# Performance work log

Hardware: AMD Instinct MI355X
Metric: run time of the kernel (lower is better)

The kernel has to match this reference:

```python
import jax, jax.numpy as jnp
import numpy as np

H = 2048      # hidden_size
I = 768       # moe_intermediate_size
E = 32        # num_experts
K = 4         # num_experts_per_tok
B, S = 1, 2048


def setup_inputs() -> dict:
    key = jax.random.key(0)
    k0, k1, k2, k3, k4 = jax.random.split(key, 5)
    return {
        "hidden_states": jax.random.normal(k0, (B, S, H), dtype=jnp.float32),
        "gate_w": jax.random.normal(k1, (E, H), dtype=jnp.float32) * 0.02,
        "Wg": jax.random.normal(k2, (E, H, I), dtype=jnp.float32) * 0.02,
        "Wu": jax.random.normal(k3, (E, H, I), dtype=jnp.float32) * 0.02,
        "Wd": jax.random.normal(k4, (E, I, H), dtype=jnp.float32) * 0.02,
        "top_k": K,
    }


def reference(hidden_states, gate_w, Wg, Wu, Wd, top_k):
    b, s, h = hidden_states.shape
    x = hidden_states.reshape(-1, h)                      # [T, H]
    T = x.shape[0]
    e = gate_w.shape[0]

    # Router: softmax over experts, then top-k and renormalize (norm_topk_prob=True)
    logits = x @ gate_w.T                                 # [T, E]
    probs = jax.nn.softmax(logits, axis=-1)
    w, sel = jax.lax.top_k(probs, top_k)                  # [T, K]
    w = w / jnp.sum(w, axis=-1, keepdims=True)

    # Scatter top-k weights into a dense [T, E] combine matrix
    combine = jnp.zeros((T, e), dtype=x.dtype).at[
        jnp.arange(T)[:, None], sel].add(w)               # [T, E]

    # Expert SiLU-gated MLPs, computed densely for all experts (mirrors the
    # ttnn path that repeats tokens across local experts and masks on combine)
    g = jnp.einsum('th,ehi->eti', x, Wg)                  # [E, T, I]
    u = jnp.einsum('th,ehi->eti', x, Wu)                  # [E, T, I]
    a = jax.nn.silu(g) * u                                # [E, T, I]
    # Fold combine weights in before the down projection to avoid an [E,T,H] temp
    a = a * combine.T[:, :, None]                         # [E, T, I]
    out = jnp.einsum('eti,eih->th', a, Wd)                # [T, H]
    return out.reshape(b, s, h)
```

## Files before the change

### kernel.cpp

```cpp
#include <hip/hip_runtime.h>
#include <cstdint>
#include <cstddef>

#define TDIM 2048
#define HDIM 2048
#define IDIM 768
#define EXP  32
#define TOPK 4
#define TKTOT 8192
#define MAXMETA 96

typedef __attribute__((ext_vector_type(8))) short short8;
typedef __attribute__((ext_vector_type(4))) float f32x4;

constexpr size_t OFF_XBF = 0;
constexpr size_t OFF_ACT = OFF_XBF + (size_t)TDIM * HDIM * 2;
constexpr size_t OFF_LOG = OFF_ACT + (size_t)TKTOT * IDIM * 2;
constexpr size_t OFF_SEL = OFF_LOG + (size_t)TDIM * EXP * 4;
constexpr size_t OFF_WTS = OFF_SEL + (size_t)TDIM * TOPK * 4;
constexpr size_t OFF_STK = OFF_WTS + (size_t)TDIM * TOPK * 4;
constexpr size_t OFF_SW  = OFF_STK + (size_t)TKTOT * 4;
constexpr size_t OFF_INV = OFF_SW  + (size_t)TKTOT * 4;
constexpr size_t OFF_CNT = OFF_INV + (size_t)TDIM * TOPK * 4;
constexpr size_t OFF_CUR = OFF_CNT + EXP * 4;
constexpr size_t OFF_OFS = OFF_CUR + EXP * 4;
constexpr size_t OFF_MET = OFF_OFS + (EXP + 1) * 4;
constexpr size_t OFF_NB  = OFF_MET + MAXMETA * 2 * 4;
constexpr size_t OFF_TMP = (OFF_NB + 4 + 255) & ~(size_t)255;
constexpr size_t TMP_BYTES = (size_t)TKTOT * HDIM * 4;
constexpr size_t WB_BYTES = (size_t)EXP * HDIM * IDIM * 2;
constexpr size_t OFF_WGB = (OFF_TMP + TMP_BYTES + 255) & ~(size_t)255;
constexpr size_t OFF_WUB = OFF_WGB + WB_BYTES;
constexpr size_t OFF_WDB = OFF_WUB + WB_BYTES;
constexpr size_t NEED_BF = OFF_WDB + WB_BYTES;

__device__ __forceinline__ unsigned short f2bf(float f) {
  unsigned u = __float_as_uint(f);
  u = (u + 0x7fffu + ((u >> 16) & 1u)) >> 16;
  return (unsigned short)u;
}
__device__ __forceinline__ unsigned pk2(float a, float b) {
  return (unsigned)f2bf(a) | ((unsigned)f2bf(b) << 16);
}
__device__ __forceinline__ void async16(void* lds, const void* g) {
  __builtin_amdgcn_global_load_lds((const __attribute__((address_space(1))) void*)g,
                                   (__attribute__((address_space(3))) void*)lds, 16, 0, 0);
}

__global__ __launch_bounds__(256) void k_cvt(const float* __restrict__ x,
                                             unsigned short* __restrict__ xb) {
  int i = blockIdx.x * 256 + threadIdx.x;
  const float4* s = (const float4*)x;
  float4 a = s[2 * i], b = s[2 * i + 1];
  uint4 o;
  o.x = pk2(a.x, a.y); o.y = pk2(a.z, a.w);
  o.z = pk2(b.x, b.y); o.w = pk2(b.z, b.w);
  ((uint4*)xb)[i] = o;
}

__global__ __launch_bounds__(256) void k_trw(const float* __restrict__ src,
                                             unsigned short* __restrict__ dst,
                                             int R, int C) {
  __shared__ float sm[64 * 65];
  int t = threadIdx.x;
  int c0 = blockIdx.x * 64, r0 = blockIdx.y * 64;
  size_t base = (size_t)blockIdx.z * R * C;
  const float* s = src + base + (size_t)r0 * C + c0;
#pragma unroll
  for (int p = 0; p < 4; p++) {
    int rl = p * 16 + (t >> 4), cl = (t & 15) * 4;
    float4 v = *(const float4*)(s + (size_t)rl * C + cl);
    float* d = &sm[rl * 65 + cl];
    d[0] = v.x; d[1] = v.y; d[2] = v.z; d[3] = v.w;
  }
  __syncthreads();
  unsigned short* o = dst + base + (size_t)c0 * R + r0;
#pragma unroll
  for (int q = 0; q < 4; q++) {
    int cl = q * 16 + (t >> 4), rq = (t & 15) * 4;
    float v0 = sm[(rq + 0) * 65 + cl], v1 = sm[(rq + 1) * 65 + cl];
    float v2 = sm[(rq + 2) * 65 + cl], v3 = sm[(rq + 3) * 65 + cl];
    uint2 u; u.x = pk2(v0, v1); u.y = pk2(v2, v3);
    *(uint2*)(o + (size_t)cl * R + rq) = u;
  }
}

__global__ __launch_bounds__(256) void k_router(const float* __restrict__ x,
                                                const float* __restrict__ gw,
                                                float* __restrict__ logits) {
  __shared__ float smx[4 * HDIM];
  int tid = threadIdx.x;
  int t0 = blockIdx.x * 4;
  const float4* src = (const float4*)(x + (size_t)t0 * HDIM);
  float4* dst = (float4*)smx;
#pragma unroll
  for (int i = 0; i < 8; i++) dst[i * 256 + tid] = src[i * 256 + tid];
  __syncthreads();
  int e = tid >> 3, sl = tid & 7;
  float acc[4] = {0.f, 0.f, 0.f, 0.f};
  const float* gptr = gw + (size_t)e * HDIM + sl * 256;
#pragma unroll 4
  for (int j = 0; j < 64; j++) {
    float4 g4 = *(const float4*)(gptr + j * 4);
#pragma unroll
    for (int tt = 0; tt < 4; tt++) {
      float4 xa = *(const float4*)&smx[tt * HDIM + sl * 256 + j * 4];
      acc[tt] += g4.x * xa.x + g4.y * xa.y + g4.z * xa.z + g4.w * xa.w;
    }
  }
  __syncthreads();
#pragma unroll
  for (int tt = 0; tt < 4; tt++) smx[(tt * EXP + e) * 8 + sl] = acc[tt];
  __syncthreads();
  if (tid < 128) {
    int tt = tid >> 5, ee = tid & 31;
    float s = 0.f;
#pragma unroll
    for (int q = 0; q < 8; q++) s += smx[(tt * EXP + ee) * 8 + q];
    logits[(size_t)(t0 + tt) * EXP + ee] = s;
  }
}

__global__ __launch_bounds__(256) void k_topk(const float* __restrict__ logits,
                                              int* __restrict__ sel,
                                              float* __restrict__ wts,
                                              int* __restrict__ cnt) {
  int t = blockIdx.x * 256 + threadIdx.x;
  float p[EXP];
  float mx = -1e30f;
#pragma unroll
  for (int e = 0; e < EXP; e++) { p[e] = logits[(size_t)t * EXP + e]; mx = fmaxf(mx, p[e]); }
#pragma unroll
  for (int e = 0; e < EXP; e++) p[e] = __expf(p[e] - mx);
  unsigned used = 0; int si[TOPK]; float sv[TOPK]; float tot = 0.f;
  for (int k = 0; k < TOPK; k++) {
    float bm = -1.f; int bi = 0;
#pragma unroll
    for (int e = 0; e < EXP; e++) {
      bool ok = !((used >> e) & 1) && (p[e] > bm);
      bm = ok ? p[e] : bm;
      bi = ok ? e : bi;
    }
    used |= 1u << bi; si[k] = bi; sv[k] = bm; tot += bm;
  }
  float inv = 1.f / tot;
#pragma unroll
  for (int k = 0; k < TOPK; k++) {
    sel[t * TOPK + k] = si[k];
    wts[t * TOPK + k] = sv[k] * inv;
    atomicAdd(&cnt[si[k]], 1);
  }
}

__global__ void k_scan(const int* __restrict__ cnt, int* __restrict__ offs,
                       int* __restrict__ cur, int* __restrict__ meta,
                       int* __restrict__ nb) {
  if (threadIdx.x == 0 && blockIdx.x == 0) {
    int off = 0, n = 0;
    for (int e = 0; e < EXP; e++) {
      offs[e] = off; cur[e] = off;
      int c = cnt[e];
      for (int r = 0; r < c && n < MAXMETA; r += 128) { meta[n * 2] = e; meta[n * 2 + 1] = r; n++; }
      off += c;
    }
    offs[EXP] = off;
    nb[0] = n;
  }
}

__global__ __launch_bounds__(256) void k_scatter(const int* __restrict__ sel,
                                                 const float* __restrict__ wts,
                                                 int* __restrict__ cur,
                                                 int* __restrict__ stok,
                                                 float* __restrict__ sw,
                                                 int* __restrict__ inv) {
  int t = blockIdx.x * 256 + threadIdx.x;
#pragma unroll
  for (int k = 0; k < TOPK; k++) {
    int e = sel[t * TOPK + k];
    int p = atomicAdd(&cur[e], 1);
    stok[p] = t;
    sw[p] = wts[t * TOPK + k];
    inv[t * TOPK + k] = p;
  }
}

__global__ __launch_bounds__(256, 3) void k_gemm1b(
    const unsigned short* __restrict__ Wgb, const unsigned short* __restrict__ Wub,
    const unsigned short* __restrict__ xb,
    const int* __restrict__ stok, const float* __restrict__ sw,
    const int* __restrict__ cnt, const int* __restrict__ offs,
    const int* __restrict__ meta, const int* __restrict__ nb,
    unsigned short* __restrict__ act) {
  int bid = blockIdx.x;
  if (bid >= nb[0]) return;
  int e = meta[bid * 2], r0 = meta[bid * 2 + 1];
  int pos0 = offs[e] + r0;
  int rows = min(128, cnt[e] - r0);
  int n0 = blockIdx.y * 64;

  __shared__ unsigned short smA[128 * 64];
  __shared__ unsigned short smBg[64 * 64];
  __shared__ unsigned short smBu[64 * 64];
  __shared__ int smTok[128];
  __shared__ float smW[128];

  int tid = threadIdx.x;
  if (tid < 128) {
    int rr = (tid < rows) ? tid : 0;
    smTok[tid] = stok[pos0 + rr];
    smW[tid] = (tid < rows) ? sw[pos0 + tid] : 0.f;
  }
  __syncthreads();

  int lane = tid & 63, w = tid >> 6;
  int waveM = w >> 1, waveN = w & 1;

  const unsigned short* aP[4];
  unsigned short* aD[4];
#pragma unroll
  for (int p = 0; p < 4; p++) {
    int r = p * 32 + w * 8 + (lane >> 3);
    aP[p] = xb + (size_t)smTok[r] * HDIM + (((lane & 7) ^ (r & 7)) << 3);
    aD[p] = &smA[(p * 32 + w * 8) * 64];
  }
  const unsigned short* gP[2]; unsigned short* gD[2];
  const unsigned short* uP[2]; unsigned short* uD[2];
  size_t wbase = (size_t)e * IDIM * HDIM;
#pragma unroll
  for (int p = 0; p < 2; p++) {
    int nr = p * 32 + w * 8 + (lane >> 3);
    size_t go = wbase + (size_t)(n0 + nr) * HDIM + (((lane & 7) ^ (nr & 7)) << 3);
    gP[p] = Wgb + go; uP[p] = Wub + go;
    gD[p] = &smBg[(p * 32 + w * 8) * 64];
    uD[p] = &smBu[(p * 32 + w * 8) * 64];
  }

  f32x4 accG[4][2], accU[4][2];
#pragma unroll
  for (int a = 0; a < 4; a++)
#pragma unroll
    for (int b = 0; b < 2; b++) { accG[a][b] = {0.f,0.f,0.f,0.f}; accU[a][b] = {0.f,0.f,0.f,0.f}; }

  int lm = lane & 15, lq = lane >> 4;

  for (int kt = 0; kt < HDIM / 64; kt++) {
    __syncthreads();
#pragma unroll
    for (int p = 0; p < 4; p++) async16(aD[p], aP[p]);
#pragma unroll
    for (int p = 0; p < 2; p++) async16(gD[p], gP[p]);
#pragma unroll
    for (int p = 0; p < 2; p++) async16(uD[p], uP[p]);
    __syncthreads();
#pragma unroll
    for (int s = 0; s < 2; s++) {
      int kq = s * 4 + lq;
      short8 af[4], bg[2], bu[2];
#pragma unroll
      for (int mt = 0; mt < 4; mt++) {
        int m = waveM * 64 + mt * 16 + lm;
        af[mt] = *(const short8*)&smA[m * 64 + ((kq ^ (m & 7)) << 3)];
      }
#pragma unroll
      for (int nt = 0; nt < 2; nt++) {
        int n = waveN * 32 + nt * 16 + lm;
        int off = n * 64 + ((kq ^ (n & 7)) << 3);
        bg[nt] = *(const short8*)&smBg[off];
        bu[nt] = *(const short8*)&smBu[off];
      }
#pragma unroll
      for (int mt = 0; mt < 4; mt++)
#pragma unroll
        for (int nt = 0; nt < 2; nt++) {
          accG[mt][nt] = __builtin_amdgcn_mfma_f32_16x16x32_bf16(af[mt], bg[nt], accG[mt][nt], 0, 0, 0);
          accU[mt][nt] = __builtin_amdgcn_mfma_f32_16x16x32_bf16(af[mt], bu[nt], accU[mt][nt], 0, 0, 0);
        }
    }
#pragma unroll
    for (int p = 0; p < 4; p++) aP[p] += 64;
#pragma unroll
    for (int p = 0; p < 2; p++) { gP[p] += 64; uP[p] += 64; }
  }

#pragma unroll
  for (int mt = 0; mt < 4; mt++)
#pragma unroll
    for (int nt = 0; nt < 2; nt++) {
      int n = n0 + waveN * 32 + nt * 16 + lm;
#pragma unroll
      for (int i = 0; i < 4; i++) {
        int r = waveM * 64 + mt * 16 + lq * 4 + i;
        if (r < rows) {
          float g = accG[mt][nt][i], u = accU[mt][nt][i];
          float sg = g / (1.f + __expf(-g));
          act[(size_t)(pos0 + r) * IDIM + n] = f2bf(sg * u * smW[r]);
        }
      }
    }
}

__global__ __launch_bounds__(256, 3) void k_gemm2b(
    const unsigned short* __restrict__ Wdb, const unsigned short* __restrict__ act,
    const int* __restrict__ cnt, const int* __restrict__ offs,
    const int* __restrict__ meta, const int* __restrict__ nb,
    float* __restrict__ tmp) {
  int bid = blockIdx.x;
  if (bid >= nb[0]) return;
  int e = meta[bid * 2], r0 = meta[bid * 2 + 1];
  int pos0 = offs[e] + r0;
  int rows = min(128, cnt[e] - r0);
  int n0 = blockIdx.y * 128;

  __shared__ unsigned short smA[128 * 64];
  __shared__ unsigned short smB[128 * 64];

  int tid = threadIdx.x;
  int lane = tid & 63, w = tid >> 6;
  int waveM = w >> 1, waveN = w & 1;

  const unsigned short* aP[4];
  unsigned short* aD[4];
#pragma unroll
  for (int p = 0; p < 4; p++) {
    int r = p * 32 + w * 8 + (lane >> 3);
    int pp = pos0 + r; if (pp > TKTOT - 1) pp = TKTOT - 1;
    aP[p] = act + (size_t)pp * IDIM + (((lane & 7) ^ (r & 7)) << 3);
    aD[p] = &smA[(p * 32 + w * 8) * 64];
  }
  const unsigned short* bP[4]; unsigned short* bD[4];
  size_t wbase = (size_t)e * IDIM * HDIM;
#pragma unroll
  for (int p = 0; p < 4; p++) {
    int nr = p * 32 + w * 8 + (lane >> 3);
    bP[p] = Wdb + wbase + (size_t)(n0 + nr) * IDIM + (((lane & 7) ^ (nr & 7)) << 3);
    bD[p] = &smB[(p * 32 + w * 8) * 64];
  }

  f32x4 acc[4][4];
#pragma unroll
  for (int a = 0; a < 4; a++)
#pragma unroll
    for (int b = 0; b < 4; b++) acc[a][b] = {0.f, 0.f, 0.f, 0.f};

  int lm = lane & 15, lq = lane >> 4;

  for (int kt = 0; kt < IDIM / 64; kt++) {
    __syncthreads();
#pragma unroll
    for (int p = 0; p < 4; p++) async16(aD[p], aP[p]);
#pragma unroll
    for (int p = 0; p < 4; p++) async16(bD[p], bP[p]);
    __syncthreads();
#pragma unroll
    for (int s = 0; s < 2; s++) {
      int kq = s * 4 + lq;
      short8 af[4], bf[4];
#pragma unroll
      for (int mt = 0; mt < 4; mt++) {
        int m = waveM * 64 + mt * 16 + lm;
        af[mt] = *(const short8*)&smA[m * 64 + ((kq ^ (m & 7)) << 3)];
      }
#pragma unroll
      for (int nt = 0; nt < 4; nt++) {
        int n = waveN * 64 + nt * 16 + lm;
        bf[nt] = *(const short8*)&smB[n * 64 + ((kq ^ (n & 7)) << 3)];
      }
#pragma unroll
      for (int mt = 0; mt < 4; mt++)
#pragma unroll
        for (int nt = 0; nt < 4; nt++)
          acc[mt][nt] = __builtin_amdgcn_mfma_f32_16x16x32_bf16(af[mt], bf[nt], acc[mt][nt], 0, 0, 0);
    }
#pragma unroll
    for (int p = 0; p < 4; p++) { aP[p] += 64; bP[p] += 64; }
  }

#pragma unroll
  for (int mt = 0; mt < 4; mt++)
#pragma unroll
    for (int nt = 0; nt < 4; nt++) {
      int n = n0 + waveN * 64 + nt * 16 + lm;
#pragma unroll
      for (int i = 0; i < 4; i++) {
        int r = waveM * 64 + mt * 16 + lq * 4 + i;
        if (r < rows) tmp[(size_t)(pos0 + r) * HDIM + n] = acc[mt][nt][i];
      }
    }
}

__global__ __launch_bounds__(256, 2) void k_gemm1(
    const float* __restrict__ Wg, const float* __restrict__ Wu,
    const unsigned short* __restrict__ xb,
    const int* __restrict__ stok, const float* __restrict__ sw,
    const int* __restrict__ cnt, const int* __restrict__ offs,
    const int* __restrict__ meta, const int* __restrict__ nb,
    unsigned short* __restrict__ act) {
  int bid = blockIdx.x;
  if (bid >= nb[0]) return;
  int e = meta[bid * 2 + 0];
  int r0 = meta[bid * 2 + 1];
  int pos0 = offs[e] + r0;
  int rows = min(128, cnt[e] - r0);
  int n0 = blockIdx.y * 128;

  __shared__ unsigned short smA[128 * 64];
  __shared__ unsigned short smBg[128 * 64];
  __shared__ unsigned short smBu[128 * 64];
  __shared__ int smTok[128];
  __shared__ float smW[128];

  int tid = threadIdx.x;
  if (tid < 128) {
    int r = tid;
    int rr = (r < rows) ? r : 0;
    smTok[r] = stok[pos0 + rr];
    smW[r] = (r < rows) ? sw[pos0 + r] : 0.f;
  }
  __syncthreads();

  int lane = tid & 63, w = tid >> 6;
  int waveM = w >> 1, waveN = w & 1;

  const unsigned short* aP[4];
  unsigned short* aD[4];
#pragma unroll
  for (int p = 0; p < 4; p++) {
    int r = p * 32 + w * 8 + (lane >> 3);
    aP[p] = xb + (size_t)smTok[r] * HDIM + (((lane & 7) ^ (r & 7)) << 3);
    aD[p] = &smA[(p * 32 + w * 8) * 64];
  }
  int bn = tid & 127, kh = tid >> 7;
  const float* pG = Wg + (size_t)e * HDIM * IDIM + (size_t)(kh * 32) * IDIM + n0 + bn;
  const float* pU = Wu + (size_t)e * HDIM * IDIM + (size_t)(kh * 32) * IDIM + n0 + bn;

  f32x4 accG[4][4], accU[4][4];
#pragma unroll
  for (int a = 0; a < 4; a++)
#pragma unroll
    for (int b = 0; b < 4; b++) { accG[a][b] = {0.f,0.f,0.f,0.f}; accU[a][b] = {0.f,0.f,0.f,0.f}; }

  int lm = lane & 15, lq = lane >> 4;

  for (int kt = 0; kt < HDIM / 64; kt++) {
    __syncthreads();
#pragma unroll
    for (int p = 0; p < 4; p++) async16(aD[p], aP[p]);
    {
      const float* q = pG; float v[32];
#pragma unroll
      for (int j = 0; j < 32; j++) { v[j] = *q; q += IDIM; }
#pragma unroll
      for (int jj = 0; jj < 4; jj++) {
        short8 o;
#pragma unroll
        for (int z = 0; z < 8; z++) o[z] = (short)f2bf(v[jj * 8 + z]);
        int ck = kh * 4 + jj;
        *(short8*)&smBg[bn * 64 + ((ck ^ (bn & 7)) << 3)] = o;
      }
    }
    {
      const float* q = pU; float v[32];
#pragma unroll
      for (int j = 0; j < 32; j++) { v[j] = *q; q += IDIM; }
#pragma unroll
      for (int jj = 0; jj < 4; jj++) {
        short8 o;
#pragma unroll
        for (int z = 0; z < 8; z++) o[z] = (short)f2bf(v[jj * 8 + z]);
        int ck = kh * 4 + jj;
        *(short8*)&smBu[bn * 64 + ((ck ^ (bn & 7)) << 3)] = o;
      }
    }
    __syncthreads();
#pragma unroll
    for (int s = 0; s < 2; s++) {
      int kq = s * 4 + lq;
      short8 af[4], bg[4], bu[4];
#pragma unroll
      for (int mt = 0; mt < 4; mt++) {
        int m = waveM * 64 + mt * 16 + lm;
        af[mt] = *(const short8*)&smA[m * 64 + ((kq ^ (m & 7)) << 3)];
      }
#pragma unroll
      for (int nt = 0; nt < 4; nt++) {
        int n = waveN * 64 + nt * 16 + lm;
        int off = n * 64 + ((kq ^ (n & 7)) << 3);
        bg[nt] = *(const short8*)&smBg[off];
        bu[nt] = *(const short8*)&smBu[off];
      }
#pragma unroll
      for (int mt = 0; mt < 4; mt++)
#pragma unroll
        for (int nt = 0; nt < 4; nt++) {
          accG[mt][nt] = __builtin_amdgcn_mfma_f32_16x16x32_bf16(af[mt], bg[nt], accG[mt][nt], 0, 0, 0);
          accU[mt][nt] = __builtin_amdgcn_mfma_f32_16x16x32_bf16(af[mt], bu[nt], accU[mt][nt], 0, 0, 0);
        }
    }
#pragma unroll
    for (int p = 0; p < 4; p++) aP[p] += 64;
    pG += (size_t)64 * IDIM;
    pU += (size_t)64 * IDIM;
  }

#pragma unroll
  for (int mt = 0; mt < 4; mt++)
#pragma unroll
    for (int nt = 0; nt < 4; nt++) {
      int n = n0 + waveN * 64 + nt * 16 + lm;
#pragma unroll
      for (int i = 0; i < 4; i++) {
        int r = waveM * 64 + mt * 16 + lq * 4 + i;
        if (r < rows) {
          float g = accG[mt][nt][i], u = accU[mt][nt][i];
          float sg = g / (1.f + __expf(-g));
          act[(size_t)(pos0 + r) * IDIM + n] = f2bf(sg * u * smW[r]);
        }
      }
    }
}

__global__ __launch_bounds__(256, 2) void k_gemm2(
    const float* __restrict__ Wd, const unsigned short* __restrict__ act,
    const int* __restrict__ stok, const int* __restrict__ cnt,
    const int* __restrict__ offs, const int* __restrict__ meta,
    const int* __restrict__ nb, float* __restrict__ dst, int mode) {
  int bid = blockIdx.x;
  if (bid >= nb[0]) return;
  int e = meta[bid * 2 + 0];
  int r0 = meta[bid * 2 + 1];
  int pos0 = offs[e] + r0;
  int rows = min(128, cnt[e] - r0);
  int n0 = blockIdx.y * 128;

  __shared__ unsigned short smA[128 * 64];
  __shared__ unsigned short smB[128 * 64];
  __shared__ int smTok[128];

  int tid = threadIdx.x;
  if (tid < 128) {
    int r = tid;
    int rr = (r < rows) ? r : 0;
    smTok[r] = stok[pos0 + rr];
  }
  __syncthreads();

  int lane = tid & 63, w = tid >> 6;
  int waveM = w >> 1, waveN = w & 1;

  const unsigned short* aP[4];
  unsigned short* aD[4];
#pragma unroll
  for (int p = 0; p < 4; p++) {
    int r = p * 32 + w * 8 + (lane >> 3);
    int pp = pos0 + r; if (pp > TKTOT - 1) pp = TKTOT - 1;
    aP[p] = act + (size_t)pp * IDIM + (((lane & 7) ^ (r & 7)) << 3);
    aD[p] = &smA[(p * 32 + w * 8) * 64];
  }
  int bn = tid & 127, kh = tid >> 7;
  const float* pD = Wd + (size_t)e * IDIM * HDIM + (size_t)(kh * 32) * HDIM + n0 + bn;

  f32x4 acc[4][4];
#pragma unroll
  for (int a = 0; a < 4; a++)
#pragma unroll
    for (int b = 0; b < 4; b++) acc[a][b] = {0.f, 0.f, 0.f, 0.f};

  int lm = lane & 15, lq = lane >> 4;

  for (int kt = 0; kt < IDIM / 64; kt++) {
    __syncthreads();
#pragma unroll
    for (int p = 0; p < 4; p++) async16(aD[p], aP[p]);
    {
      const float* q = pD; float v[32];
#pragma unroll
      for (int j = 0; j < 32; j++) { v[j] = *q; q += HDIM; }
#pragma unroll
      for (int jj = 0; jj < 4; jj++) {
        short8 o;
#pragma unroll
        for (int z = 0; z < 8; z++) o[z] = (short)f2bf(v[jj * 8 + z]);
        int ck = kh * 4 + jj;
        *(short8*)&smB[bn * 64 + ((ck ^ (bn & 7)) << 3)] = o;
      }
    }
    __syncthreads();
#pragma unroll
    for (int s = 0; s < 2; s++) {
      int kq = s * 4 + lq;
      short8 af[4], bf[4];
#pragma unroll
      for (int mt = 0; mt < 4; mt++) {
        int m = waveM * 64 + mt * 16 + lm;
        af[mt] = *(const short8*)&smA[m * 64 + ((kq ^ (m & 7)) << 3)];
      }
#pragma unroll
      for (int nt = 0; nt < 4; nt++) {
        int n = waveN * 64 + nt * 16 + lm;
        bf[nt] = *(const short8*)&smB[n * 64 + ((kq ^ (n & 7)) << 3)];
      }
#pragma unroll
      for (int mt = 0; mt < 4; mt++)
#pragma unroll
        for (int nt = 0; nt < 4; nt++)
          acc[mt][nt] = __builtin_amdgcn_mfma_f32_16x16x32_bf16(af[mt], bf[nt], acc[mt][nt], 0, 0, 0);
    }
#pragma unroll
    for (int p = 0; p < 4; p++) aP[p] += 64;
    pD += (size_t)64 * HDIM;
  }

#pragma unroll
  for (int mt = 0; mt < 4; mt++)
#pragma unroll
    for (int nt = 0; nt < 4; nt++) {
      int n = n0 + waveN * 64 + nt * 16 + lm;
#pragma unroll
      for (int i = 0; i < 4; i++) {
        int r = waveM * 64 + mt * 16 + lq * 4 + i;
        if (r < rows) {
          float val = acc[mt][nt][i];
          if (mode == 0) {
            dst[(size_t)(pos0 + r) * HDIM + n] = val;
          } else {
            __hip_atomic_fetch_add(&dst[(size_t)smTok[r] * HDIM + n], val,
                                   __ATOMIC_RELAXED, __HIP_MEMORY_SCOPE_AGENT);
          }
        }
      }
    }
}

__global__ __launch_bounds__(256) void k_reduce(const float* __restrict__ tmp,
                                                const int* __restrict__ inv,
                                                float* __restrict__ out) {
  int u = blockIdx.x * 256 + threadIdx.x;
  int t = u >> 9, c = u & 511;
  int i0 = inv[t * 4 + 0], i1 = inv[t * 4 + 1], i2 = inv[t * 4 + 2], i3 = inv[t * 4 + 3];
  float4 a = *(const float4*)(tmp + (size_t)i0 * HDIM + c * 4);
  float4 b = *(const float4*)(tmp + (size_t)i1 * HDIM + c * 4);
  float4 d = *(const float4*)(tmp + (size_t)i2 * HDIM + c * 4);
  float4 e = *(const float4*)(tmp + (size_t)i3 * HDIM + c * 4);
  float4 s;
  s.x = a.x + b.x + d.x + e.x;
  s.y = a.y + b.y + d.y + e.y;
  s.z = a.z + b.z + d.z + e.z;
  s.w = a.w + b.w + d.w + e.w;
  *(float4*)(out + (size_t)t * HDIM + c * 4) = s;
}

extern "C" void kernel_launch(void* const* d_in, const int* in_sizes, int n_in,
                              void* d_out, int out_size, void* d_ws, size_t ws_size,
                              hipStream_t stream) {
  const float* x  = (const float*)d_in[0];
  const float* gw = (const float*)d_in[1];
  const float* Wg = (const float*)d_in[2];
  const float* Wu = (const float*)d_in[3];
  const float* Wd = (const float*)d_in[4];
  float* out = (float*)d_out;

  char* ws = (char*)d_ws;
  unsigned short* xb  = (unsigned short*)(ws + OFF_XBF);
  unsigned short* act = (unsigned short*)(ws + OFF_ACT);
  float* logits = (float*)(ws + OFF_LOG);
  int*   sel    = (int*)(ws + OFF_SEL);
  float* wts    = (float*)(ws + OFF_WTS);
  int*   stok   = (int*)(ws + OFF_STK);
  float* sw     = (float*)(ws + OFF_SW);
  int*   inv    = (int*)(ws + OFF_INV);
  int*   cnt    = (int*)(ws + OFF_CNT);
  int*   cur    = (int*)(ws + OFF_CUR);
  int*   offs   = (int*)(ws + OFF_OFS);
  int*   meta   = (int*)(ws + OFF_MET);
  int*   nb     = (int*)(ws + OFF_NB);
  float* tmp    = (float*)(ws + OFF_TMP);
  unsigned short* Wgb = (unsigned short*)(ws + OFF_WGB);
  unsigned short* Wub = (unsigned short*)(ws + OFF_WUB);
  unsigned short* Wdb = (unsigned short*)(ws + OFF_WDB);

  bool useTmp = ws_size >= OFF_TMP + TMP_BYTES;
  bool useBF  = ws_size >= NEED_BF;

  hipMemsetAsync(cnt, 0, EXP * 4, stream);
  k_cvt<<<(TDIM * HDIM / 8) / 256, 256, 0, stream>>>(x, xb);
  k_router<<<TDIM / 4, 256, 0, stream>>>(x, gw, logits);
  k_topk<<<TDIM / 256, 256, 0, stream>>>(logits, sel, wts, cnt);
  k_scan<<<1, 64, 0, stream>>>(cnt, offs, cur, meta, nb);
  k_scatter<<<TDIM / 256, 256, 0, stream>>>(sel, wts, cur, stok, sw, inv);

  if (useBF) {
    k_trw<<<dim3(IDIM / 64, HDIM / 64, EXP), 256, 0, stream>>>(Wg, Wgb, HDIM, IDIM);
    k_trw<<<dim3(IDIM / 64, HDIM / 64, EXP), 256, 0, stream>>>(Wu, Wub, HDIM, IDIM);
    k_trw<<<dim3(HDIM / 64, IDIM / 64, EXP), 256, 0, stream>>>(Wd, Wdb, IDIM, HDIM);
    k_gemm1b<<<dim3(MAXMETA, IDIM / 64), 256, 0, stream>>>(Wgb, Wub, xb, stok, sw, cnt, offs, meta, nb, act);
    k_gemm2b<<<dim3(MAXMETA, HDIM / 128), 256, 0, stream>>>(Wdb, act, cnt, offs, meta, nb, tmp);
    k_reduce<<<(TDIM * 512) / 256, 256, 0, stream>>>(tmp, inv, out);
  } else {
    k_gemm1<<<dim3(MAXMETA, IDIM / 128), 256, 0, stream>>>(Wg, Wu, xb, stok, sw, cnt, offs, meta, nb, act);
    if (useTmp) {
      k_gemm2<<<dim3(MAXMETA, HDIM / 128), 256, 0, stream>>>(Wd, act, stok, cnt, offs, meta, nb, tmp, 0);
      k_reduce<<<(TDIM * 512) / 256, 256, 0, stream>>>(tmp, inv, out);
    } else {
      hipMemsetAsync(out, 0, (size_t)TDIM * HDIM * 4, stream);
      k_gemm2<<<dim3(MAXMETA, HDIM / 128), 256, 0, stream>>>(Wd, act, stok, cnt, offs, meta, nb, out, 1);
    }
  }
}
```

Baseline: 828.4 us.

## Drop weight pre-transpose; stream fp32 weights into double-buffered 256-row expert GEMMs

Removes the per-call kernels that transposed all expert weights to bf16 in workspace. The two grouped GEMMs now read fp32 weights directly and convert them to bf16 in registers. Both GEMMs get double-buffered LDS, with the next tile's loads issued before the current tile's MFMAs. Tiles grow to 256 tokens with 512-thread blocks, and block indices are remapped. The aim is to cut the extra full pass over weight memory and to hide load latency, at the cost of uncoalesced strided fp32 weight loads, more register and LDS pressure, and one block per CU.

```diff
diff --git a/kernel.cpp b/kernel.cpp
--- a/kernel.cpp
+++ b/kernel.cpp
@@ -9,6 +9,8 @@
 #define TOPK 4
 #define TKTOT 8192
 #define MAXMETA 96
+#define CHUNK 256
+#define NMETA 64
 
 typedef __attribute__((ext_vector_type(8))) short short8;
 typedef __attribute__((ext_vector_type(4))) float f32x4;
@@ -28,11 +30,6 @@
 constexpr size_t OFF_NB  = OFF_MET + MAXMETA * 2 * 4;
 constexpr size_t OFF_TMP = (OFF_NB + 4 + 255) & ~(size_t)255;
 constexpr size_t TMP_BYTES = (size_t)TKTOT * HDIM * 4;
-constexpr size_t WB_BYTES = (size_t)EXP * HDIM * IDIM * 2;
-constexpr size_t OFF_WGB = (OFF_TMP + TMP_BYTES + 255) & ~(size_t)255;
-constexpr size_t OFF_WUB = OFF_WGB + WB_BYTES;
-constexpr size_t OFF_WDB = OFF_WUB + WB_BYTES;
-constexpr size_t NEED_BF = OFF_WDB + WB_BYTES;
 
 __device__ __forceinline__ unsigned short f2bf(float f) {
   unsigned u = __float_as_uint(f);
@@ -58,33 +55,6 @@
   ((uint4*)xb)[i] = o;
 }
 
-__global__ __launch_bounds__(256) void k_trw(const float* __restrict__ src,
-                                             unsigned short* __restrict__ dst,
-                                             int R, int C) {
-  __shared__ float sm[64 * 65];
-  int t = threadIdx.x;
-  int c0 = blockIdx.x * 64, r0 = blockIdx.y * 64;
-  size_t base = (size_t)blockIdx.z * R * C;
-  const float* s = src + base + (size_t)r0 * C + c0;
-#pragma unroll
-  for (int p = 0; p < 4; p++) {
-    int rl = p * 16 + (t >> 4), cl = (t & 15) * 4;
-    float4 v = *(const float4*)(s + (size_t)rl * C + cl);
-    float* d = &sm[rl * 65 + cl];
-    d[0] = v.x; d[1] = v.y; d[2] = v.z; d[3] = v.w;
-  }
-  __syncthreads();
-  unsigned short* o = dst + base + (size_t)c0 * R + r0;
-#pragma unroll
-  for (int q = 0; q < 4; q++) {
-    int cl = q * 16 + (t >> 4), rq = (t & 15) * 4;
-    float v0 = sm[(rq + 0) * 65 + cl], v1 = sm[(rq + 1) * 65 + cl];
-    float v2 = sm[(rq + 2) * 65 + cl], v3 = sm[(rq + 3) * 65 + cl];
-    uint2 u; u.x = pk2(v0, v1); u.y = pk2(v2, v3);
-    *(uint2*)(o + (size_t)cl * R + rq) = u;
-  }
-}
-
 __global__ __launch_bounds__(256) void k_router(const float* __restrict__ x,
                                                 const float* __restrict__ gw,
                                                 float* __restrict__ logits) {
@@ -160,7 +130,7 @@
     for (int e = 0; e < EXP; e++) {
       offs[e] = off; cur[e] = off;
       int c = cnt[e];
-      for (int r = 0; r < c && n < MAXMETA; r += 128) { meta[n * 2] = e; meta[n * 2 + 1] = r; n++; }
+      for (int r = 0; r < c && n < NMETA; r += CHUNK) { meta[n * 2] = e; meta[n * 2 + 1] = r; n++; }
       off += c;
     }
     offs[EXP] = off;
@@ -185,28 +155,28 @@
   }
 }
 
-__global__ __launch_bounds__(256, 3) void k_gemm1b(
-    const unsigned short* __restrict__ Wgb, const unsigned short* __restrict__ Wub,
+__global__ __launch_bounds__(512, 1) void k_gemm1n(
+    const float* __restrict__ Wg, const float* __restrict__ Wu,
     const unsigned short* __restrict__ xb,
     const int* __restrict__ stok, const float* __restrict__ sw,
     const int* __restrict__ cnt, const int* __restrict__ offs,
     const int* __restrict__ meta, const int* __restrict__ nb,
     unsigned short* __restrict__ act) {
-  int bid = blockIdx.x;
+  int bid = (blockIdx.x & 7) * 8 + (blockIdx.x >> 3);
   if (bid >= nb[0]) return;
   int e = meta[bid * 2], r0 = meta[bid * 2 + 1];
   int pos0 = offs[e] + r0;
-  int rows = min(128, cnt[e] - r0);
+  int rows = min(CHUNK, cnt[e] - r0);
   int n0 = blockIdx.y * 64;
 
-  __shared__ unsigned short smA[128 * 64];
-  __shared__ unsigned short smBg[64 * 64];
-  __shared__ unsigned short smBu[64 * 64];
-  __shared__ int smTok[128];
-  __shared__ float smW[128];
+  __shared__ unsigned short smA[2][CHUNK * 64];
+  __shared__ unsigned short smBg[2][64 * 64];
+  __shared__ unsigned short smBu[2][64 * 64];
+  __shared__ int smTok[CHUNK];
+  __shared__ float smW[CHUNK];
 
   int tid = threadIdx.x;
-  if (tid < 128) {
+  if (tid < CHUNK) {
     int rr = (tid < rows) ? tid : 0;
     smTok[tid] = stok[pos0 + rr];
     smW[tid] = (tid < rows) ? sw[pos0 + tid] : 0.f;
@@ -216,25 +186,17 @@
   int lane = tid & 63, w = tid >> 6;
   int waveM = w >> 1, waveN = w & 1;
 
-  const unsigned short* aP[4];
-  unsigned short* aD[4];
+  const unsigned short* aC[4];
 #pragma unroll
   for (int p = 0; p < 4; p++) {
-    int r = p * 32 + w * 8 + (lane >> 3);
-    aP[p] = xb + (size_t)smTok[r] * HDIM + (((lane & 7) ^ (r & 7)) << 3);
-    aD[p] = &smA[(p * 32 + w * 8) * 64];
-  }
-  const unsigned short* gP[2]; unsigned short* gD[2];
-  const unsigned short* uP[2]; unsigned short* uD[2];
-  size_t wbase = (size_t)e * IDIM * HDIM;
-#pragma unroll
-  for (int p = 0; p < 2; p++) {
-    int nr = p * 32 + w * 8 + (lane >> 3);
-    size_t go = wbase + (size_t)(n0 + nr) * HDIM + (((lane & 7) ^ (nr & 7)) << 3);
-    gP[p] = Wgb + go; uP[p] = Wub + go;
-    gD[p] = &smBg[(p * 32 + w * 8) * 64];
-    uD[p] = &smBu[(p * 32 + w * 8) * 64];
-  }
+    int r = p * 64 + w * 8 + (lane >> 3);
+    aC[p] = xb + (size_t)smTok[r] * HDIM + (((lane & 7) ^ (r & 7)) << 3);
+  }
+  size_t wb = (size_t)e * HDIM * IDIM;
+  int bn = tid & 63, kh = tid >> 6;
+  const float* pG = Wg + wb + (size_t)(kh * 8) * IDIM + n0 + bn;
+  const float* pU = Wu + wb + (size_t)(kh * 8) * IDIM + n0 + bn;
+  int bOff = bn * 64 + ((kh ^ (bn & 7)) << 3);
 
   f32x4 accG[4][2], accU[4][2];
 #pragma unroll
@@ -243,16 +205,31 @@
     for (int b = 0; b < 2; b++) { accG[a][b] = {0.f,0.f,0.f,0.f}; accU[a][b] = {0.f,0.f,0.f,0.f}; }
 
   int lm = lane & 15, lq = lane >> 4;
-
-  for (int kt = 0; kt < HDIM / 64; kt++) {
-    __syncthreads();
-#pragma unroll
-    for (int p = 0; p < 4; p++) async16(aD[p], aP[p]);
-#pragma unroll
-    for (int p = 0; p < 2; p++) async16(gD[p], gP[p]);
-#pragma unroll
-    for (int p = 0; p < 2; p++) async16(uD[p], uP[p]);
-    __syncthreads();
+  float vg[8], vu[8];
+
+#pragma unroll
+  for (int p = 0; p < 4; p++) async16(&smA[0][(p * 64 + w * 8) * 64], aC[p]);
+#pragma unroll
+  for (int j = 0; j < 8; j++) { vg[j] = pG[(size_t)j * IDIM]; vu[j] = pU[(size_t)j * IDIM]; }
+  {
+    short8 og, ou;
+#pragma unroll
+    for (int z = 0; z < 8; z++) { og[z] = (short)f2bf(vg[z]); ou[z] = (short)f2bf(vu[z]); }
+    *(short8*)&smBg[0][bOff] = og;
+    *(short8*)&smBu[0][bOff] = ou;
+  }
+  __syncthreads();
+
+  const int NK = HDIM / 64;
+  for (int kt = 0; kt < NK; kt++) {
+    int c = kt & 1;
+    if (kt + 1 < NK) {
+#pragma unroll
+      for (int p = 0; p < 4; p++) { aC[p] += 64; async16(&smA[c ^ 1][(p * 64 + w * 8) * 64], aC[p]); }
+      pG += (size_t)64 * IDIM; pU += (size_t)64 * IDIM;
+#pragma unroll
+      for (int j = 0; j < 8; j++) { vg[j] = pG[(size_t)j * IDIM]; vu[j] = pU[(size_t)j * IDIM]; }
+    }
 #pragma unroll
     for (int s = 0; s < 2; s++) {
       int kq = s * 4 + lq;
@@ -260,14 +237,14 @@
 #pragma unroll
       for (int mt = 0; mt < 4; mt++) {
         int m = waveM * 64 + mt * 16 + lm;
-        af[mt] = *(const short8*)&smA[m * 64 + ((kq ^ (m & 7)) << 3)];
+        af[mt] = *(const short8*)&smA[c][m * 64 + ((kq ^ (m & 7)) << 3)];
       }
 #pragma unroll
       for (int nt = 0; nt < 2; nt++) {
         int n = waveN * 32 + nt * 16 + lm;
         int off = n * 64 + ((kq ^ (n & 7)) << 3);
-        bg[nt] = *(const short8*)&smBg[off];
-        bu[nt] = *(const short8*)&smBu[off];
+        bg[nt] = *(const short8*)&smBg[c][off];
+        bu[nt] = *(const short8*)&smBu[c][off];
       }
 #pragma unroll
       for (int mt = 0; mt < 4; mt++)
@@ -277,10 +254,14 @@
           accU[mt][nt] = __builtin_amdgcn_mfma_f32_16x16x32_bf16(af[mt], bu[nt], accU[mt][nt], 0, 0, 0);
         }
     }
-#pragma unroll
-    for (int p = 0; p < 4; p++) aP[p] += 64;
-#pragma unroll
-    for (int p = 0; p < 2; p++) { gP[p] += 64; uP[p] += 64; }
+    if (kt + 1 < NK) {
+      short8 og, ou;
+#pragma unroll
+      for (int z = 0; z < 8; z++) { og[z] = (short)f2bf(vg[z]); ou[z] = (short)f2bf(vu[z]); }
+      *(short8*)&smBg[c ^ 1][bOff] = og;
+      *(short8*)&smBu[c ^ 1][bOff] = ou;
+    }
+    __syncthreads();
   }
 
 #pragma unroll
@@ -300,265 +281,42 @@
     }
 }
 
-__global__ __launch_bounds__(256, 3) void k_gemm2b(
-    const unsigned short* __restrict__ Wdb, const unsigned short* __restrict__ act,
-    const int* __restrict__ cnt, const int* __restrict__ offs,
-    const int* __restrict__ meta, const int* __restrict__ nb,
-    float* __restrict__ tmp) {
-  int bid = blockIdx.x;
-  if (bid >= nb[0]) return;
-  int e = meta[bid * 2], r0 = meta[bid * 2 + 1];
-  int pos0 = offs[e] + r0;
-  int rows = min(128, cnt[e] - r0);
-  int n0 = blockIdx.y * 128;
-
-  __shared__ unsigned short smA[128 * 64];
-  __shared__ unsigned short smB[128 * 64];
-
-  int tid = threadIdx.x;
-  int lane = tid & 63, w = tid >> 6;
-  int waveM = w >> 1, waveN = w & 1;
-
-  const unsigned short* aP[4];
-  unsigned short* aD[4];
-#pragma unroll
-  for (int p = 0; p < 4; p++) {
-    int r = p * 32 + w * 8 + (lane >> 3);
-    int pp = pos0 + r; if (pp > TKTOT - 1) pp = TKTOT - 1;
-    aP[p] = act + (size_t)pp * IDIM + (((lane & 7) ^ (r & 7)) << 3);
-    aD[p] = &smA[(p * 32 + w * 8) * 64];
-  }
-  const unsigned short* bP[4]; unsigned short* bD[4];
-  size_t wbase = (size_t)e * IDIM * HDIM;
-#pragma unroll
-  for (int p = 0; p < 4; p++) {
-    int nr = p * 32 + w * 8 + (lane >> 3);
-    bP[p] = Wdb + wbase + (size_t)(n0 + nr) * IDIM + (((lane & 7) ^ (nr & 7)) << 3);
-    bD[p] = &smB[(p * 32 + w * 8) * 64];
-  }
-
-  f32x4 acc[4][4];
-#pragma unroll
-  for (int a = 0; a < 4; a++)
-#pragma unroll
-    for (int b = 0; b < 4; b++) acc[a][b] = {0.f, 0.f, 0.f, 0.f};
-
-  int lm = lane & 15, lq = lane >> 4;
-
-  for (int kt = 0; kt < IDIM / 64; kt++) {
-    __syncthreads();
-#pragma unroll
-    for (int p = 0; p < 4; p++) async16(aD[p], aP[p]);
-#pragma unroll
-    for (int p = 0; p < 4; p++) async16(bD[p], bP[p]);
-    __syncthreads();
-#pragma unroll
-    for (int s = 0; s < 2; s++) {
-      int kq = s * 4 + lq;
-      short8 af[4], bf[4];
-#pragma unroll
-      for (int mt = 0; mt < 4; mt++) {
-        int m = waveM * 64 + mt * 16 + lm;
-        af[mt] = *(const short8*)&smA[m * 64 + ((kq ^ (m & 7)) << 3)];
-      }
-#pragma unroll
-      for (int nt = 0; nt < 4; nt++) {
-        int n = waveN * 64 + nt * 16 + lm;
-        bf[nt] = *(const short8*)&smB[n * 64 + ((kq ^ (n & 7)) << 3)];
-      }
-#pragma unroll
-      for (int mt = 0; mt < 4; mt++)
-#pragma unroll
-        for (int nt = 0; nt < 4; nt++)
-          acc[mt][nt] = __builtin_amdgcn_mfma_f32_16x16x32_bf16(af[mt], bf[nt], acc[mt][nt], 0, 0, 0);
-    }
-#pragma unroll
-    for (int p = 0; p < 4; p++) { aP[p] += 64; bP[p] += 64; }
-  }
-
-#pragma unroll
-  for (int mt = 0; mt < 4; mt++)
-#pragma unroll
-    for (int nt = 0; nt < 4; nt++) {
-      int n = n0 + waveN * 64 + nt * 16 + lm;
-#pragma unroll
-      for (int i = 0; i < 4; i++) {
-        int r = waveM * 64 + mt * 16 + lq * 4 + i;
-        if (r < rows) tmp[(size_t)(pos0 + r) * HDIM + n] = acc[mt][nt][i];
-      }
-    }
-}
-
-__global__ __launch_bounds__(256, 2) void k_gemm1(
-    const float* __restrict__ Wg, const float* __restrict__ Wu,
-    const unsigned short* __restrict__ xb,
-    const int* __restrict__ stok, const float* __restrict__ sw,
-    const int* __restrict__ cnt, const int* __restrict__ offs,
-    const int* __restrict__ meta, const int* __restrict__ nb,
-    unsigned short* __restrict__ act) {
-  int bid = blockIdx.x;
-  if (bid >= nb[0]) return;
-  int e = meta[bid * 2 + 0];
-  int r0 = meta[bid * 2 + 1];
-  int pos0 = offs[e] + r0;
-  int rows = min(128, cnt[e] - r0);
-  int n0 = blockIdx.y * 128;
-
-  __shared__ unsigned short smA[128 * 64];
-  __shared__ unsigned short smBg[128 * 64];
-  __shared__ unsigned short smBu[128 * 64];
-  __shared__ int smTok[128];
-  __shared__ float smW[128];
-
-  int tid = threadIdx.x;
-  if (tid < 128) {
-    int r = tid;
-    int rr = (r < rows) ? r : 0;
-    smTok[r] = stok[pos0 + rr];
-    smW[r] = (r < rows) ? sw[pos0 + r] : 0.f;
-  }
-  __syncthreads();
-
-  int lane = tid & 63, w = tid >> 6;
-  int waveM = w >> 1, waveN = w & 1;
-
-  const unsigned short* aP[4];
-  unsigned short* aD[4];
-#pragma unroll
-  for (int p = 0; p < 4; p++) {
-    int r = p * 32 + w * 8 + (lane >> 3);
-    aP[p] = xb + (size_t)smTok[r] * HDIM + (((lane & 7) ^ (r & 7)) << 3);
-    aD[p] = &smA[(p * 32 + w * 8) * 64];
-  }
-  int bn = tid & 127, kh = tid >> 7;
-  const float* pG = Wg + (size_t)e * HDIM * IDIM + (size_t)(kh * 32) * IDIM + n0 + bn;
-  const float* pU = Wu + (size_t)e * HDIM * IDIM + (size_t)(kh * 32) * IDIM + n0 + bn;
-
-  f32x4 accG[4][4], accU[4][4];
-#pragma unroll
-  for (int a = 0; a < 4; a++)
-#pragma unroll
-    for (int b = 0; b < 4; b++) { accG[a][b] = {0.f,0.f,0.f,0.f}; accU[a][b] = {0.f,0.f,0.f,0.f}; }
-
-  int lm = lane & 15, lq = lane >> 4;
-
-  for (int kt = 0; kt < HDIM / 64; kt++) {
-    __syncthreads();
-#pragma unroll
-    for (int p = 0; p < 4; p++) async16(aD[p], aP[p]);
-    {
-      const float* q = pG; float v[32];
-#pragma unroll
-      for (int j = 0; j < 32; j++) { v[j] = *q; q += IDIM; }
-#pragma unroll
-      for (int jj = 0; jj < 4; jj++) {
-        short8 o;
-#pragma unroll
-        for (int z = 0; z < 8; z++) o[z] = (short)f2bf(v[jj * 8 + z]);
-        int ck = kh * 4 + jj;
-        *(short8*)&smBg[bn * 64 + ((ck ^ (bn & 7)) << 3)] = o;
-      }
-    }
-    {
-      const float* q = pU; float v[32];
-#pragma unroll
-      for (int j = 0; j < 32; j++) { v[j] = *q; q += IDIM; }
-#pragma unroll
-      for (int jj = 0; jj < 4; jj++) {
-        short8 o;
-#pragma unroll
-        for (int z = 0; z < 8; z++) o[z] = (short)f2bf(v[jj * 8 + z]);
-        int ck = kh * 4 + jj;
-        *(short8*)&smBu[bn * 64 + ((ck ^ (bn & 7)) << 3)] = o;
-      }
-    }
-    __syncthreads();
-#pragma unroll
-    for (int s = 0; s < 2; s++) {
-      int kq = s * 4 + lq;
-      short8 af[4], bg[4], bu[4];
-#pragma unroll
-      for (int mt = 0; mt < 4; mt++) {
-        int m = waveM * 64 + mt * 16 + lm;
-        af[mt] = *(const short8*)&smA[m * 64 + ((kq ^ (m & 7)) << 3)];
-      }
-#pragma unroll
-      for (int nt = 0; nt < 4; nt++) {
-        int n = waveN * 64 + nt * 16 + lm;
-        int off = n * 64 + ((kq ^ (n & 7)) << 3);
-        bg[nt] = *(const short8*)&smBg[off];
-        bu[nt] = *(const short8*)&smBu[off];
-      }
-#pragma unroll
-      for (int mt = 0; mt < 4; mt++)
-#pragma unroll
-        for (int nt = 0; nt < 4; nt++) {
-          accG[mt][nt] = __builtin_amdgcn_mfma_f32_16x16x32_bf16(af[mt], bg[nt], accG[mt][nt], 0, 0, 0);
-          accU[mt][nt] = __builtin_amdgcn_mfma_f32_16x16x32_bf16(af[mt], bu[nt], accU[mt][nt], 0, 0, 0);
-        }
-    }
-#pragma unroll
-    for (int p = 0; p < 4; p++) aP[p] += 64;
-    pG += (size_t)64 * IDIM;
-    pU += (size_t)64 * IDIM;
-  }
-
-#pragma unroll
-  for (int mt = 0; mt < 4; mt++)
-#pragma unroll
-    for (int nt = 0; nt < 4; nt++) {
-      int n = n0 + waveN * 64 + nt * 16 + lm;
-#pragma unroll
-      for (int i = 0; i < 4; i++) {
-        int r = waveM * 64 + mt * 16 + lq * 4 + i;
-        if (r < rows) {
-          float g = accG[mt][nt][i], u = accU[mt][nt][i];
-          float sg = g / (1.f + __expf(-g));
-          act[(size_t)(pos0 + r) * IDIM + n] = f2bf(sg * u * smW[r]);
-        }
-      }
-    }
-}
-
-__global__ __launch_bounds__(256, 2) void k_gemm2(
+__global__ __launch_bounds__(512, 1) void k_gemm2n(
     const float* __restrict__ Wd, const unsigned short* __restrict__ act,
     const int* __restrict__ stok, const int* __restrict__ cnt,
     const int* __restrict__ offs, const int* __restrict__ meta,
     const int* __restrict__ nb, float* __restrict__ dst, int mode) {
-  int bid = blockIdx.x;
+  int bid = (blockIdx.x & 7) * 8 + (blockIdx.x >> 3);
   if (bid >= nb[0]) return;
-  int e = meta[bid * 2 + 0];
-  int r0 = meta[bid * 2 + 1];
+  int e = meta[bid * 2], r0 = meta[bid * 2 + 1];
   int pos0 = offs[e] + r0;
-  int rows = min(128, cnt[e] - r0);
+  int rows = min(CHUNK, cnt[e] - r0);
   int n0 = blockIdx.y * 128;
 
-  __shared__ unsigned short smA[128 * 64];
-  __shared__ unsigned short smB[128 * 64];
-  __shared__ int smTok[128];
+  __shared__ unsigned short smA[2][CHUNK * 64];
+  __shared__ unsigned short smB[2][128 * 64];
+  __shared__ int smTok[CHUNK];
 
   int tid = threadIdx.x;
-  if (tid < 128) {
-    int r = tid;
-    int rr = (r < rows) ? r : 0;
-    smTok[r] = stok[pos0 + rr];
+  if (tid < CHUNK) {
+    int rr = (tid < rows) ? tid : 0;
+    smTok[tid] = stok[pos0 + rr];
   }
   __syncthreads();
 
   int lane = tid & 63, w = tid >> 6;
   int waveM = w >> 1, waveN = w & 1;
 
-  const unsigned short* aP[4];
-  unsigned short* aD[4];
+  const unsigned short* aC[4];
 #pragma unroll
   for (int p = 0; p < 4; p++) {
-    int r = p * 32 + w * 8 + (lane >> 3);
+    int r = p * 64 + w * 8 + (lane >> 3);
     int pp = pos0 + r; if (pp > TKTOT - 1) pp = TKTOT - 1;
-    aP[p] = act + (size_t)pp * IDIM + (((lane & 7) ^ (r & 7)) << 3);
-    aD[p] = &smA[(p * 32 + w * 8) * 64];
-  }
+    aC[p] = act + (size_t)pp * IDIM + (((lane & 7) ^ (r & 7)) << 3);
+  }
+  size_t wb = (size_t)e * IDIM * HDIM;
   int bn = tid & 127, kh = tid >> 7;
-  const float* pD = Wd + (size_t)e * IDIM * HDIM + (size_t)(kh * 32) * HDIM + n0 + bn;
+  const float* pD = Wd + wb + (size_t)(kh * 16) * HDIM + n0 + bn;
 
   f32x4 acc[4][4];
 #pragma unroll
@@ -567,25 +325,31 @@
     for (int b = 0; b < 4; b++) acc[a][b] = {0.f, 0.f, 0.f, 0.f};
 
   int lm = lane & 15, lq = lane >> 4;
-
-  for (int kt = 0; kt < IDIM / 64; kt++) {
-    __syncthreads();
-#pragma unroll
-    for (int p = 0; p < 4; p++) async16(aD[p], aP[p]);
-    {
-      const float* q = pD; float v[32];
-#pragma unroll
-      for (int j = 0; j < 32; j++) { v[j] = *q; q += HDIM; }
-#pragma unroll
-      for (int jj = 0; jj < 4; jj++) {
-        short8 o;
-#pragma unroll
-        for (int z = 0; z < 8; z++) o[z] = (short)f2bf(v[jj * 8 + z]);
-        int ck = kh * 4 + jj;
-        *(short8*)&smB[bn * 64 + ((ck ^ (bn & 7)) << 3)] = o;
-      }
-    }
-    __syncthreads();
+  float v[16];
+
+#pragma unroll
+  for (int p = 0; p < 4; p++) async16(&smA[0][(p * 64 + w * 8) * 64], aC[p]);
+#pragma unroll
+  for (int j = 0; j < 16; j++) v[j] = pD[(size_t)j * HDIM];
+#pragma unroll
+  for (int jj = 0; jj < 2; jj++) {
+    short8 o;
+#pragma unroll
+    for (int z = 0; z < 8; z++) o[z] = (short)f2bf(v[jj * 8 + z]);
+    *(short8*)&smB[0][bn * 64 + (((kh * 2 + jj) ^ (bn & 7)) << 3)] = o;
+  }
+  __syncthreads();
+
+  const int NK = IDIM / 64;
+  for (int kt = 0; kt < NK; kt++) {
+    int c = kt & 1;
+    if (kt + 1 < NK) {
+#pragma unroll
+      for (int p = 0; p < 4; p++) { aC[p] += 64; async16(&smA[c ^ 1][(p * 64 + w * 8) * 64], aC[p]); }
+      pD += (size_t)64 * HDIM;
+#pragma unroll
+      for (int j = 0; j < 16; j++) v[j] = pD[(size_t)j * HDIM];
+    }
 #pragma unroll
     for (int s = 0; s < 2; s++) {
       int kq = s * 4 + lq;
@@ -593,12 +357,12 @@
 #pragma unroll
       for (int mt = 0; mt < 4; mt++) {
         int m = waveM * 64 + mt * 16 + lm;
-        af[mt] = *(const short8*)&smA[m * 64 + ((kq ^ (m & 7)) << 3)];
+        af[mt] = *(const short8*)&smA[c][m * 64 + ((kq ^ (m & 7)) << 3)];
       }
 #pragma unroll
       for (int nt = 0; nt < 4; nt++) {
         int n = waveN * 64 + nt * 16 + lm;
-        bf[nt] = *(const short8*)&smB[n * 64 + ((kq ^ (n & 7)) << 3)];
+        bf[nt] = *(const short8*)&smB[c][n * 64 + ((kq ^ (n & 7)) << 3)];
       }
 #pragma unroll
       for (int mt = 0; mt < 4; mt++)
@@ -606,9 +370,16 @@
         for (int nt = 0; nt < 4; nt++)
           acc[mt][nt] = __builtin_amdgcn_mfma_f32_16x16x32_bf16(af[mt], bf[nt], acc[mt][nt], 0, 0, 0);
     }
-#pragma unroll
-    for (int p = 0; p < 4; p++) aP[p] += 64;
-    pD += (size_t)64 * HDIM;
+    if (kt + 1 < NK) {
+#pragma unroll
+      for (int jj = 0; jj < 2; jj++) {
+        short8 o;
+#pragma unroll
+        for (int z = 0; z < 8; z++) o[z] = (short)f2bf(v[jj * 8 + z]);
+        *(short8*)&smB[c ^ 1][bn * 64 + (((kh * 2 + jj) ^ (bn & 7)) << 3)] = o;
+      }
+    }
+    __syncthreads();
   }
 
 #pragma unroll
@@ -675,12 +446,8 @@
   int*   meta   = (int*)(ws + OFF_MET);
   int*   nb     = (int*)(ws + OFF_NB);
   float* tmp    = (float*)(ws + OFF_TMP);
-  unsigned short* Wgb = (unsigned short*)(ws + OFF_WGB);
-  unsigned short* Wub = (unsigned short*)(ws + OFF_WUB);
-  unsigned short* Wdb = (unsigned short*)(ws + OFF_WDB);
 
   bool useTmp = ws_size >= OFF_TMP + TMP_BYTES;
-  bool useBF  = ws_size >= NEED_BF;
 
   hipMemsetAsync(cnt, 0, EXP * 4, stream);
   k_cvt<<<(TDIM * HDIM / 8) / 256, 256, 0, stream>>>(x, xb);
@@ -689,21 +456,12 @@
   k_scan<<<1, 64, 0, stream>>>(cnt, offs, cur, meta, nb);
   k_scatter<<<TDIM / 256, 256, 0, stream>>>(sel, wts, cur, stok, sw, inv);
 
-  if (useBF) {
-    k_trw<<<dim3(IDIM / 64, HDIM / 64, EXP), 256, 0, stream>>>(Wg, Wgb, HDIM, IDIM);
-    k_trw<<<dim3(IDIM / 64, HDIM / 64, EXP), 256, 0, stream>>>(Wu, Wub, HDIM, IDIM);
-    k_trw<<<dim3(HDIM / 64, IDIM / 64, EXP), 256, 0, stream>>>(Wd, Wdb, IDIM, HDIM);
-    k_gemm1b<<<dim3(MAXMETA, IDIM / 64), 256, 0, stream>>>(Wgb, Wub, xb, stok, sw, cnt, offs, meta, nb, act);
-    k_gemm2b<<<dim3(MAXMETA, HDIM / 128), 256, 0, stream>>>(Wdb, act, cnt, offs, meta, nb, tmp);
+  k_gemm1n<<<dim3(NMETA, IDIM / 64), 512, 0, stream>>>(Wg, Wu, xb, stok, sw, cnt, offs, meta, nb, act);
+  if (useTmp) {
+    k_gemm2n<<<dim3(NMETA, HDIM / 128), 512, 0, stream>>>(Wd, act, stok, cnt, offs, meta, nb, tmp, 0);
     k_reduce<<<(TDIM * 512) / 256, 256, 0, stream>>>(tmp, inv, out);
   } else {
-    k_gemm1<<<dim3(MAXMETA, IDIM / 128), 256, 0, stream>>>(Wg, Wu, xb, stok, sw, cnt, offs, meta, nb, act);
-    if (useTmp) {
-      k_gemm2<<<dim3(MAXMETA, HDIM / 128), 256, 0, stream>>>(Wd, act, stok, cnt, offs, meta, nb, tmp, 0);
-      k_reduce<<<(TDIM * 512) / 256, 256, 0, stream>>>(tmp, inv, out);
-    } else {
-      hipMemsetAsync(out, 0, (size_t)TDIM * HDIM * 4, stream);
-      k_gemm2<<<dim3(MAXMETA, HDIM / 128), 256, 0, stream>>>(Wd, act, stok, cnt, offs, meta, nb, out, 1);
-    }
-  }
-}
+    hipMemsetAsync(out, 0, (size_t)TDIM * HDIM * 4, stream);
+    k_gemm2n<<<dim3(NMETA, HDIM / 128), 512, 0, stream>>>(Wd, act, stok, cnt, offs, meta, nb, out, 1);
+  }
+}
```

Measured after the change: 806.5 us. 2.6% less time.
